# Kernel optimization log

Hardware: AMD Instinct MI355X
Metric: run time of the kernel (lower is better)

Reference implementation:

```python
import jax, jax.numpy as jnp
import numpy as np

NUM_EDGES = 10000
NUM_PATHS = 30000
MAX_LEN = 16
LINK_DIM = 128
PATH_DIM = 128


def setup_inputs() -> dict:
    key = jax.random.key(0)
    k0, k1, k2, k3, k4, k5, k6, k7 = jax.random.split(key, 8)
    inputs = jax.random.normal(k0, (NUM_EDGES, LINK_DIM), dtype=jnp.float32)
    # every path has exactly MAX_LEN hops -> unique (path, pos) scatter indices
    idx = jnp.repeat(jnp.arange(NUM_PATHS, dtype=jnp.int64), MAX_LEN)
    seqs = jnp.tile(jnp.arange(MAX_LEN, dtype=jnp.int64), NUM_PATHS)
    paths = jax.random.randint(k1, (NUM_PATHS * MAX_LEN,), 0, NUM_EDGES).astype(jnp.int64)
    # GRU params (Keras GRUCell, reset_after=True): kernel [D,3U], recurrent [U,3U], two bias rows
    s_in = 1.0 / np.sqrt(LINK_DIM)
    s_h = 1.0 / np.sqrt(PATH_DIM)
    kernel = jax.random.uniform(k2, (LINK_DIM, 3 * PATH_DIM), minval=-s_in, maxval=s_in, dtype=jnp.float32)
    rec_kernel = jax.random.uniform(k3, (PATH_DIM, 3 * PATH_DIM), minval=-s_h, maxval=s_h, dtype=jnp.float32)
    bias_i = jnp.zeros((3 * PATH_DIM,), dtype=jnp.float32)
    bias_r = jnp.zeros((3 * PATH_DIM,), dtype=jnp.float32)
    wq = jax.random.uniform(k4, (PATH_DIM, PATH_DIM), minval=-s_h, maxval=s_h, dtype=jnp.float32)
    wk = jax.random.uniform(k5, (PATH_DIM, PATH_DIM), minval=-s_h, maxval=s_h, dtype=jnp.float32)
    wv = jax.random.uniform(k6, (PATH_DIM, PATH_DIM), minval=-s_h, maxval=s_h, dtype=jnp.float32)
    return {"inputs": inputs, "paths": paths, "idx": idx, "seqs": seqs,
            "kernel": kernel, "rec_kernel": rec_kernel, "bias_i": bias_i, "bias_r": bias_r,
            "wq": wq, "wk": wk, "wv": wv}


def _gru_scan(link_inputs, kernel, rec_kernel, bias_i, bias_r):
    # link_inputs: [P, L, D] -> hidden_states [P, L, U], last_state [P, U]
    U = rec_kernel.shape[0]
    P = link_inputs.shape[0]
    xs = jnp.transpose(link_inputs, (1, 0, 2))  # [L, P, D]

    def step(h, x):
        xm = x @ kernel + bias_i          # [P, 3U]
        hm = h @ rec_kernel + bias_r      # [P, 3U]  (reset_after=True)
        xz, xr, xh = xm[:, :U], xm[:, U:2 * U], xm[:, 2 * U:]
        hz, hr, hh = hm[:, :U], hm[:, U:2 * U], hm[:, 2 * U:]
        z = jax.nn.sigmoid(xz + hz)
        r = jax.nn.sigmoid(xr + hr)
        cand = jnp.tanh(xh + r * hh)
        h_new = z * h + (1.0 - z) * cand
        return h_new, h_new

    h0 = jnp.zeros((P, U), dtype=link_inputs.dtype)
    last, hs = jax.lax.scan(step, h0, xs)
    return jnp.transpose(hs, (1, 0, 2)), last  # [P, L, U], [P, U]


def reference(inputs, paths, idx, seqs, kernel, rec_kernel, bias_i, bias_r, wq, wk, wv):
    h_tild = inputs[paths]  # gather: [P*L, D]
    link_inputs = jnp.zeros((NUM_PATHS, MAX_LEN, LINK_DIM), dtype=inputs.dtype)
    link_inputs = link_inputs.at[idx, seqs].set(h_tild)  # scatter_nd
    hidden_states, last_state = _gru_scan(link_inputs, kernel, rec_kernel, bias_i, bias_r)
    key = jnp.einsum('plu,uv->plv', hidden_states, wk)
    query = last_state @ wq                     # [P, U]
    value = jnp.einsum('plu,uv->plv', hidden_states, wv)
    att = jnp.einsum('plv,pv->pl', key, query)  # raw scores, no softmax (faithful)
    context = jnp.einsum('pl,plv->pv', att, value)[:, None, :]  # [P, 1, U]
    return context
```

## Files before the change

kernel.cpp:

```cpp
#include <hip/hip_runtime.h>


#define NUM_PATHS 30000
#define T 16
#define NTILES 1875
#define NPAIRS 938
#define NEDGES 10000

typedef float f32x4 __attribute__((ext_vector_type(4)));
typedef short bf16x8 __attribute__((ext_vector_type(8)));

__device__ __forceinline__ short f2bf(float f) {
    union { float f; unsigned u; } v; v.f = f;
    return (short)((v.u + 0x8000u) >> 16);
}
__device__ __forceinline__ float bf2f(short s) {
    union { unsigned u; float f; } v; v.u = ((unsigned)(unsigned short)s) << 16;
    return v.f;
}
__device__ __forceinline__ float fsig(float x) {
    return __builtin_amdgcn_rcpf(1.0f + __expf(-x));
}
__device__ __forceinline__ float ftanhf_(float x) {
    return 1.0f - 2.0f * __builtin_amdgcn_rcpf(1.0f + __expf(2.0f * x));
}

#define MFMA(a, b, c) __builtin_amdgcn_mfma_f32_16x16x32_bf16((a), (b), (c), 0, 0, 0)

#define GRU_T 12288
#define QK_T 16384
#define WV_T 2048
__global__ void prep_kernel(const float* __restrict__ Wx, const float* __restrict__ Wr,
                            const float* __restrict__ wq, const float* __restrict__ wk,
                            const float* __restrict__ wv,
                            short* __restrict__ wpk) {
    int id = blockIdx.x * 256 + threadIdx.x;
    if (id < GRU_T) {
        int f = id >> 9, rem = id & 511;
        int w = rem >> 6, lane = rem & 63;
        int quad = lane >> 4, c16 = lane & 15;
        int col = 16 * w + c16;
        short o[8];
        #pragma unroll
        for (int j = 0; j < 8; ++j) {
            float v;
            if (f < 16) {
                int k = (f & 7) * 32 + quad * 8 + j;
                int cc = col + ((f < 8) ? 0 : 128);
                v = (k < 128) ? Wx[k * 384 + cc] : Wr[(k - 128) * 384 + cc];
            } else {
                int k = ((f - 16) & 3) * 32 + quad * 8 + j;
                v = (f < 20) ? Wx[k * 384 + 256 + col] : Wr[k * 384 + 256 + col];
            }
            o[j] = f2bf(v);
        }
        *(bf16x8*)&wpk[id * 8] = *(bf16x8*)o;
        return;
    }
    if (id < GRU_T + QK_T) {
        int t2 = id - GRU_T;
        int j = t2 & 7, lane = (t2 >> 3) & 63, w = (t2 >> 9) & 7, kc = t2 >> 12;
        int quad = lane >> 4, c16 = lane & 15, col = 16 * w + c16;
        int k = kc * 32 + quad * 8 + j;
        const float* qr = wq + k * 128;
        const float* kr = wk + col * 128;
        float s = 0.f;
        #pragma unroll 8
        for (int vv = 0; vv < 128; ++vv) s += qr[vv] * kr[vv];
        short hi = f2bf(s);
        wpk[(((24 + kc) * 8 + w) * 64 + lane) * 8 + j] = hi;
        wpk[(((28 + kc) * 8 + w) * 64 + lane) * 8 + j] = f2bf(s - bf2f(hi));
        return;
    }
    if (id < GRU_T + QK_T + WV_T) {
        int t2 = id - GRU_T - QK_T;
        int lane = t2 & 63, w = (t2 >> 6) & 7, kc = t2 >> 9;
        int quad = lane >> 4, c16 = lane & 15, col = 16 * w + c16;
        short hi8[8], lo8[8];
        #pragma unroll
        for (int j = 0; j < 8; ++j) {
            float v = wv[(kc * 32 + quad * 8 + j) * 128 + col];
            hi8[j] = f2bf(v);
            lo8[j] = f2bf(v - bf2f(hi8[j]));
        }
        *(bf16x8*)&wpk[(((32 + kc) * 8 + w) * 64 + lane) * 8] = *(bf16x8*)hi8;
        *(bf16x8*)&wpk[(((36 + kc) * 8 + w) * 64 + lane) * 8] = *(bf16x8*)lo8;
    }
}

__global__ __launch_bounds__(512) void eprep_kernel(
    const float* __restrict__ inputs, const short* __restrict__ wpk,
    uint2* __restrict__ E8) {
    const int w = threadIdx.x >> 6, lane = threadIdx.x & 63;
    const int quad = lane >> 4, c16 = lane & 15;
    const int ucol = 16 * w + c16;
    const int e0 = blockIdx.x * 16;

    bf16x8 A[4];
    const float* row = inputs + (e0 + c16) * 128;
    #pragma unroll
    for (int kc = 0; kc < 4; ++kc) {
        float4 a = *(const float4*)&row[kc * 32 + quad * 8];
        float4 b = *(const float4*)&row[kc * 32 + quad * 8 + 4];
        short o[8] = {f2bf(a.x), f2bf(a.y), f2bf(a.z), f2bf(a.w),
                      f2bf(b.x), f2bf(b.y), f2bf(b.z), f2bf(b.w)};
        A[kc] = *(bf16x8*)o;
    }
    f32x4 az = {0.f, 0.f, 0.f, 0.f}, ar = az, ax = az;
    #pragma unroll
    for (int kc = 0; kc < 4; ++kc) {
        bf16x8 Bz = *(const bf16x8*)&wpk[(((0 + kc) * 8 + w) * 64 + lane) * 8];
        bf16x8 Br = *(const bf16x8*)&wpk[(((8 + kc) * 8 + w) * 64 + lane) * 8];
        bf16x8 Bx = *(const bf16x8*)&wpk[(((16 + kc) * 8 + w) * 64 + lane) * 8];
        az = MFMA(A[kc], Bz, az);
        ar = MFMA(A[kc], Br, ar);
        ax = MFMA(A[kc], Bx, ax);
    }
    #pragma unroll
    for (int r = 0; r < 4; ++r) {
        unsigned zr = (unsigned)(unsigned short)f2bf(az[r]) |
                      ((unsigned)(unsigned short)f2bf(ar[r]) << 16);
        uint2 val;
        val.x = zr;
        val.y = __float_as_uint(ax[r]);
        E8[(e0 + quad * 4 + r) * 128 + ucol] = val;
    }
}

#define ROWS 136
#define HSLOT 2184

__global__ __launch_bounds__(512, 2) void path_emb_kernel(
    const int* __restrict__ paths, const short* __restrict__ wpk,
    const uint2* __restrict__ E8,
    const float* __restrict__ bias_i, const float* __restrict__ bias_r,
    float* __restrict__ out)
{
    __shared__ __align__(16) short s_hist[2][16][HSLOT];
    __shared__ __align__(16) short s_xb[2][2][T * ROWS];
    __shared__ float s_att[2][16][20];

    const int tid  = threadIdx.x;
    const int w    = tid >> 6;
    const int lane = tid & 63;
    const int quad = lane >> 4;
    const int c16  = lane & 15;
    const int ucol = 16 * w + c16;

    const float bz  = bias_i[ucol] + bias_r[ucol];
    const float brr = bias_i[128 + ucol] + bias_r[128 + ucol];
    const float bxh = bias_i[256 + ucol];
    const float bhh = bias_r[256 + ucol];

    bf16x8 Bzh[4], Brh[4], Bhh[4];
    #pragma unroll
    for (int kc = 0; kc < 4; ++kc) {
        Bzh[kc] = *(const bf16x8*)&wpk[(((4 + kc)  * 8 + w) * 64 + lane) * 8];
        Brh[kc] = *(const bf16x8*)&wpk[(((12 + kc) * 8 + w) * 64 + lane) * 8];
        Bhh[kc] = *(const bf16x8*)&wpk[(((20 + kc) * 8 + w) * 64 + lane) * 8];
    }

    for (int pi = blockIdx.x; pi < NPAIRS; pi += gridDim.x) {
        const int tA = 2 * pi;
        const int tB = (2 * pi + 1 < NTILES) ? 2 * pi + 1 : NTILES - 1;
        const int p0A = tA * T, p0B = tB * T;

        float hA[4] = {0.f, 0.f, 0.f, 0.f}, hB[4] = {0.f, 0.f, 0.f, 0.f};

        uint2 Ea[8], Eb[8];
        {
            int e0i[8];
            #pragma unroll
            for (int i = 0; i < 4; ++i) {
                e0i[i]     = paths[(p0A + quad * 4 + i) * 16];
                e0i[4 + i] = paths[(p0B + quad * 4 + i) * 16];
            }
            #pragma unroll
            for (int i = 0; i < 8; ++i) Ea[i] = E8[e0i[i] * 128 + ucol];
        }

        auto window = [&](int t, uint2* Ecur, uint2* Enext) {
            __syncthreads();

            if (t < 15) {
                int en[8];
                #pragma unroll
                for (int i = 0; i < 4; ++i) {
                    en[i]     = paths[(p0A + quad * 4 + i) * 16 + t + 1];
                    en[4 + i] = paths[(p0B + quad * 4 + i) * 16 + t + 1];
                }
                #pragma unroll
                for (int i = 0; i < 8; ++i) Enext[i] = E8[en[i] * 128 + ucol];
            }

            f32x4 azA = {bz, bz, bz, bz},     azB = azA;
            f32x4 arA = {brr, brr, brr, brr}, arB = arA;
            f32x4 achA = {bhh, bhh, bhh, bhh}, achB = achA;

            if (t > 0) {
                bf16x8 ahA[4], ahB[4];
                #pragma unroll
                for (int kc = 0; kc < 4; ++kc) {
                    ahA[kc] = *(const bf16x8*)&s_hist[0][t - 1][c16 * ROWS + kc * 32 + quad * 8];
                    ahB[kc] = *(const bf16x8*)&s_hist[1][t - 1][c16 * ROWS + kc * 32 + quad * 8];
                }
                #pragma unroll
                for (int kc = 0; kc < 4; ++kc) {
                    azA  = MFMA(ahA[kc], Bzh[kc], azA);
                    azB  = MFMA(ahB[kc], Bzh[kc], azB);
                    arA  = MFMA(ahA[kc], Brh[kc], arA);
                    arB  = MFMA(ahB[kc], Brh[kc], arB);
                    achA = MFMA(ahA[kc], Bhh[kc], achA);
                    achB = MFMA(ahB[kc], Bhh[kc], achB);
                }
            }

            #pragma unroll
            for (int r = 0; r < 4; ++r) {
                float zx = __uint_as_float(Ecur[r].x << 16);
                float rx = __uint_as_float(Ecur[r].x & 0xffff0000u);
                float xh = __uint_as_float(Ecur[r].y);
                float z    = fsig(azA[r] + zx);
                float rr   = fsig(arA[r] + rx);
                float cand = ftanhf_(xh + bxh + rr * achA[r]);
                hA[r] = cand + z * (hA[r] - cand);
                s_hist[0][t][(quad * 4 + r) * ROWS + ucol] = f2bf(hA[r]);
            }
            #pragma unroll
            for (int r = 0; r < 4; ++r) {
                float zx = __uint_as_float(Ecur[4 + r].x << 16);
                float rx = __uint_as_float(Ecur[4 + r].x & 0xffff0000u);
                float xh = __uint_as_float(Ecur[4 + r].y);
                float z    = fsig(azB[r] + zx);
                float rr   = fsig(arB[r] + rx);
                float cand = ftanhf_(xh + bxh + rr * achB[r]);
                hB[r] = cand + z * (hB[r] - cand);
                s_hist[1][t][(quad * 4 + r) * ROWS + ucol] = f2bf(hB[r]);
            }
        };

        #pragma unroll 1
        for (int t2 = 0; t2 < 8; ++t2) {
            window(2 * t2,     Ea, Eb);
            window(2 * t2 + 1, Eb, Ea);
        }

        #pragma unroll
        for (int r = 0; r < 4; ++r) {
            float hf = hA[r]; short hi = f2bf(hf);
            s_xb[0][0][(quad * 4 + r) * ROWS + ucol] = f2bf(hf - bf2f(hi));
            hf = hB[r]; hi = f2bf(hf);
            s_xb[1][0][(quad * 4 + r) * ROWS + ucol] = f2bf(hf - bf2f(hi));
        }
        __syncthreads();

        f32x4 uA = {0.f, 0.f, 0.f, 0.f}, uB = uA;
        #pragma unroll
        for (int kc = 0; kc < 4; ++kc) {
            bf16x8 bqh = *(const bf16x8*)&wpk[(((24 + kc) * 8 + w) * 64 + lane) * 8];
            bf16x8 bql = *(const bf16x8*)&wpk[(((28 + kc) * 8 + w) * 64 + lane) * 8];
            bf16x8 AhA = *(const bf16x8*)&s_hist[0][15][c16 * ROWS + kc * 32 + quad * 8];
            bf16x8 AlA = *(const bf16x8*)&s_xb[0][0][c16 * ROWS + kc * 32 + quad * 8];
            bf16x8 AhB = *(const bf16x8*)&s_hist[1][15][c16 * ROWS + kc * 32 + quad * 8];
            bf16x8 AlB = *(const bf16x8*)&s_xb[1][0][c16 * ROWS + kc * 32 + quad * 8];
            uA = MFMA(AhA, bqh, uA); uA = MFMA(AhA, bql, uA); uA = MFMA(AlA, bqh, uA);
            uB = MFMA(AhB, bqh, uB); uB = MFMA(AhB, bql, uB); uB = MFMA(AlB, bqh, uB);
        }
        __syncthreads();

        #pragma unroll
        for (int r = 0; r < 4; ++r) {
            int off = (quad * 4 + r) * ROWS + ucol;
            float v = uA[r]; short hi = f2bf(v);
            s_xb[0][0][off] = hi; s_xb[0][1][off] = f2bf(v - bf2f(hi));
            v = uB[r]; hi = f2bf(v);
            s_xb[1][0][off] = hi; s_xb[1][1][off] = f2bf(v - bf2f(hi));
        }
        __syncthreads();

        {
            int et = tid >> 8, p = (tid >> 4) & 15, l = tid & 15;
            const short* uh = &s_xb[et][0][p * ROWS];
            const short* ul = &s_xb[et][1][p * ROWS];
            const short* hh = &s_hist[et][l][p * ROWS];
            float a = 0.f;
            #pragma unroll
            for (int u8 = 0; u8 < 128; u8 += 8) {
                bf16x8 vh = *(const bf16x8*)&uh[u8];
                bf16x8 vl = *(const bf16x8*)&ul[u8];
                bf16x8 vt = *(const bf16x8*)&hh[u8];
                #pragma unroll
                for (int j = 0; j < 8; ++j)
                    a += (bf2f(vh[j]) + bf2f(vl[j])) * bf2f(vt[j]);
            }
            s_att[et][p][l] = a;
        }
        __syncthreads();

        {
            int et = tid >> 8, p = (tid >> 4) & 15, v0 = (tid & 15) * 8;
            float ctx[8];
            #pragma unroll
            for (int j = 0; j < 8; ++j) ctx[j] = 0.f;
            #pragma unroll
            for (int l = 0; l < 16; ++l) {
                float al = s_att[et][p][l];
                bf16x8 hv = *(const bf16x8*)&s_hist[et][l][p * ROWS + v0];
                #pragma unroll
                for (int j = 0; j < 8; ++j) ctx[j] += al * bf2f(hv[j]);
            }
            #pragma unroll
            for (int j = 0; j < 8; ++j) {
                short hi = f2bf(ctx[j]);
                s_xb[et][0][p * ROWS + v0 + j] = hi;
                s_xb[et][1][p * ROWS + v0 + j] = f2bf(ctx[j] - bf2f(hi));
            }
        }
        __syncthreads();

        f32x4 oA = {0.f, 0.f, 0.f, 0.f}, oB = oA;
        #pragma unroll
        for (int kc = 0; kc < 4; ++kc) {
            bf16x8 bwh = *(const bf16x8*)&wpk[(((32 + kc) * 8 + w) * 64 + lane) * 8];
            bf16x8 bwl = *(const bf16x8*)&wpk[(((36 + kc) * 8 + w) * 64 + lane) * 8];
            bf16x8 AhA = *(const bf16x8*)&s_xb[0][0][c16 * ROWS + kc * 32 + quad * 8];
            bf16x8 AlA = *(const bf16x8*)&s_xb[0][1][c16 * ROWS + kc * 32 + quad * 8];
            bf16x8 AhB = *(const bf16x8*)&s_xb[1][0][c16 * ROWS + kc * 32 + quad * 8];
            bf16x8 AlB = *(const bf16x8*)&s_xb[1][1][c16 * ROWS + kc * 32 + quad * 8];
            oA = MFMA(AhA, bwh, oA); oA = MFMA(AhA, bwl, oA); oA = MFMA(AlA, bwh, oA);
            oB = MFMA(AhB, bwh, oB); oB = MFMA(AhB, bwl, oB); oB = MFMA(AlB, bwh, oB);
        }
        #pragma unroll
        for (int r = 0; r < 4; ++r) {
            out[(p0A + quad * 4 + r) * 128 + ucol] = oA[r];
            out[(p0B + quad * 4 + r) * 128 + ucol] = oB[r];
        }
    }
}

extern "C" void kernel_launch(void* const* d_in, const int* in_sizes, int n_in,
                              void* d_out, int out_size, void* d_ws, size_t ws_size,
                              hipStream_t stream) {
    const float* inputs = (const float*)d_in[0];
    const int*   paths  = (const int*)d_in[1];
    const float* wx  = (const float*)d_in[4];
    const float* wr  = (const float*)d_in[5];
    const float* bi  = (const float*)d_in[6];
    const float* br  = (const float*)d_in[7];
    const float* wq  = (const float*)d_in[8];
    const float* wk  = (const float*)d_in[9];
    const float* wvp = (const float*)d_in[10];

    char* ws = (char*)d_ws;
    uint2* E8 = (uint2*)ws;
    short* wpk = (short*)(ws + 10240000);

    int prep_n = GRU_T + QK_T + WV_T;
    prep_kernel<<<(prep_n + 255) / 256, 256, 0, stream>>>(wx, wr, wq, wk, wvp, wpk);
    eprep_kernel<<<NEDGES / 16, 512, 0, stream>>>(inputs, wpk, E8);
    path_emb_kernel<<<256, 512, 0, stream>>>(paths, wpk, E8, bi, br, (float*)d_out);
}
```

Baseline: 221.0 us.

## Process one 16-path tile per block and raise occupancy to four blocks per CU

```diff
diff --git a/kernel.cpp b/kernel.cpp
--- a/kernel.cpp
+++ b/kernel.cpp
@@ -4,11 +4,11 @@
 #define NUM_PATHS 30000
 #define T 16
 #define NTILES 1875
-#define NPAIRS 938
 #define NEDGES 10000
 
 typedef float f32x4 __attribute__((ext_vector_type(4)));
 typedef short bf16x8 __attribute__((ext_vector_type(8)));
+typedef short bf16x4 __attribute__((ext_vector_type(4)));
 
 __device__ __forceinline__ short f2bf(float f) {
     union { float f; unsigned u; } v; v.f = f;
@@ -130,14 +130,14 @@
 #define ROWS 136
 #define HSLOT 2184
 
-__global__ __launch_bounds__(512, 2) void path_emb_kernel(
+__global__ __launch_bounds__(512, 4) void path_emb_kernel(
     const int* __restrict__ paths, const short* __restrict__ wpk,
     const uint2* __restrict__ E8,
     const float* __restrict__ bias_i, const float* __restrict__ bias_r,
     float* __restrict__ out)
 {
-    __shared__ __align__(16) short s_hist[2][16][HSLOT];
-    __shared__ __align__(16) short s_xb[2][2][T * ROWS];
+    __shared__ __align__(16) short s_hist[16][HSLOT];
+    __shared__ __align__(16) short s_xb[2][T * ROWS];
     __shared__ float s_att[2][16][20];
 
     const int tid  = threadIdx.x;
@@ -160,182 +160,144 @@
         Bhh[kc] = *(const bf16x8*)&wpk[(((20 + kc) * 8 + w) * 64 + lane) * 8];
     }
 
-    for (int pi = blockIdx.x; pi < NPAIRS; pi += gridDim.x) {
-        const int tA = 2 * pi;
-        const int tB = (2 * pi + 1 < NTILES) ? 2 * pi + 1 : NTILES - 1;
-        const int p0A = tA * T, p0B = tB * T;
-
-        float hA[4] = {0.f, 0.f, 0.f, 0.f}, hB[4] = {0.f, 0.f, 0.f, 0.f};
-
-        uint2 Ea[8], Eb[8];
-        {
-            int e0i[8];
-            #pragma unroll
-            for (int i = 0; i < 4; ++i) {
-                e0i[i]     = paths[(p0A + quad * 4 + i) * 16];
-                e0i[4 + i] = paths[(p0B + quad * 4 + i) * 16];
+    const int p0 = blockIdx.x * T;
+
+    float hA[4] = {0.f, 0.f, 0.f, 0.f};
+
+    uint2 Ea[4], Eb[4];
+    {
+        int e0i[4];
+        #pragma unroll
+        for (int i = 0; i < 4; ++i)
+            e0i[i] = paths[(p0 + quad * 4 + i) * 16];
+        #pragma unroll
+        for (int i = 0; i < 4; ++i) Ea[i] = E8[e0i[i] * 128 + ucol];
+    }
+
+    auto window = [&](int t, uint2* Ecur, uint2* Enext) {
+        __syncthreads();
+
+        if (t < 15) {
+            int en[4];
+            #pragma unroll
+            for (int i = 0; i < 4; ++i)
+                en[i] = paths[(p0 + quad * 4 + i) * 16 + t + 1];
+            #pragma unroll
+            for (int i = 0; i < 4; ++i) Enext[i] = E8[en[i] * 128 + ucol];
+        }
+
+        f32x4 az  = {bz, bz, bz, bz};
+        f32x4 ar  = {brr, brr, brr, brr};
+        f32x4 ach = {bhh, bhh, bhh, bhh};
+
+        if (t > 0) {
+            bf16x8 ah[4];
+            #pragma unroll
+            for (int kc = 0; kc < 4; ++kc)
+                ah[kc] = *(const bf16x8*)&s_hist[t - 1][c16 * ROWS + kc * 32 + quad * 8];
+            #pragma unroll
+            for (int kc = 0; kc < 4; ++kc) {
+                az  = MFMA(ah[kc], Bzh[kc], az);
+                ar  = MFMA(ah[kc], Brh[kc], ar);
+                ach = MFMA(ah[kc], Bhh[kc], ach);
             }
-            #pragma unroll
-            for (int i = 0; i < 8; ++i) Ea[i] = E8[e0i[i] * 128 + ucol];
-        }
-
-        auto window = [&](int t, uint2* Ecur, uint2* Enext) {
-            __syncthreads();
-
-            if (t < 15) {
-                int en[8];
-                #pragma unroll
-                for (int i = 0; i < 4; ++i) {
-                    en[i]     = paths[(p0A + quad * 4 + i) * 16 + t + 1];
-                    en[4 + i] = paths[(p0B + quad * 4 + i) * 16 + t + 1];
-                }
-                #pragma unroll
-                for (int i = 0; i < 8; ++i) Enext[i] = E8[en[i] * 128 + ucol];
-            }
-
-            f32x4 azA = {bz, bz, bz, bz},     azB = azA;
-            f32x4 arA = {brr, brr, brr, brr}, arB = arA;
-            f32x4 achA = {bhh, bhh, bhh, bhh}, achB = achA;
-
-            if (t > 0) {
-                bf16x8 ahA[4], ahB[4];
-                #pragma unroll
-                for (int kc = 0; kc < 4; ++kc) {
-                    ahA[kc] = *(const bf16x8*)&s_hist[0][t - 1][c16 * ROWS + kc * 32 + quad * 8];
-                    ahB[kc] = *(const bf16x8*)&s_hist[1][t - 1][c16 * ROWS + kc * 32 + quad * 8];
-                }
-                #pragma unroll
-                for (int kc = 0; kc < 4; ++kc) {
-                    azA  = MFMA(ahA[kc], Bzh[kc], azA);
-                    azB  = MFMA(ahB[kc], Bzh[kc], azB);
-                    arA  = MFMA(ahA[kc], Brh[kc], arA);
-                    arB  = MFMA(ahB[kc], Brh[kc], arB);
-                    achA = MFMA(ahA[kc], Bhh[kc], achA);
-                    achB = MFMA(ahB[kc], Bhh[kc], achB);
-                }
-            }
-
-            #pragma unroll
-            for (int r = 0; r < 4; ++r) {
-                float zx = __uint_as_float(Ecur[r].x << 16);
-                float rx = __uint_as_float(Ecur[r].x & 0xffff0000u);
-                float xh = __uint_as_float(Ecur[r].y);
-                float z    = fsig(azA[r] + zx);
-                float rr   = fsig(arA[r] + rx);
-                float cand = ftanhf_(xh + bxh + rr * achA[r]);
-                hA[r] = cand + z * (hA[r] - cand);
-                s_hist[0][t][(quad * 4 + r) * ROWS + ucol] = f2bf(hA[r]);
-            }
-            #pragma unroll
-            for (int r = 0; r < 4; ++r) {
-                float zx = __uint_as_float(Ecur[4 + r].x << 16);
-                float rx = __uint_as_float(Ecur[4 + r].x & 0xffff0000u);
-                float xh = __uint_as_float(Ecur[4 + r].y);
-                float z    = fsig(azB[r] + zx);
-                float rr   = fsig(arB[r] + rx);
-                float cand = ftanhf_(xh + bxh + rr * achB[r]);
-                hB[r] = cand + z * (hB[r] - cand);
-                s_hist[1][t][(quad * 4 + r) * ROWS + ucol] = f2bf(hB[r]);
-            }
-        };
-
-        #pragma unroll 1
-        for (int t2 = 0; t2 < 8; ++t2) {
-            window(2 * t2,     Ea, Eb);
-            window(2 * t2 + 1, Eb, Ea);
         }
 
         #pragma unroll
         for (int r = 0; r < 4; ++r) {
-            float hf = hA[r]; short hi = f2bf(hf);
-            s_xb[0][0][(quad * 4 + r) * ROWS + ucol] = f2bf(hf - bf2f(hi));
-            hf = hB[r]; hi = f2bf(hf);
-            s_xb[1][0][(quad * 4 + r) * ROWS + ucol] = f2bf(hf - bf2f(hi));
-        }
-        __syncthreads();
-
-        f32x4 uA = {0.f, 0.f, 0.f, 0.f}, uB = uA;
-        #pragma unroll
-        for (int kc = 0; kc < 4; ++kc) {
-            bf16x8 bqh = *(const bf16x8*)&wpk[(((24 + kc) * 8 + w) * 64 + lane) * 8];
-            bf16x8 bql = *(const bf16x8*)&wpk[(((28 + kc) * 8 + w) * 64 + lane) * 8];
-            bf16x8 AhA = *(const bf16x8*)&s_hist[0][15][c16 * ROWS + kc * 32 + quad * 8];
-            bf16x8 AlA = *(const bf16x8*)&s_xb[0][0][c16 * ROWS + kc * 32 + quad * 8];
-            bf16x8 AhB = *(const bf16x8*)&s_hist[1][15][c16 * ROWS + kc * 32 + quad * 8];
-            bf16x8 AlB = *(const bf16x8*)&s_xb[1][0][c16 * ROWS + kc * 32 + quad * 8];
-            uA = MFMA(AhA, bqh, uA); uA = MFMA(AhA, bql, uA); uA = MFMA(AlA, bqh, uA);
-            uB = MFMA(AhB, bqh, uB); uB = MFMA(AhB, bql, uB); uB = MFMA(AlB, bqh, uB);
-        }
-        __syncthreads();
-
-        #pragma unroll
-        for (int r = 0; r < 4; ++r) {
-            int off = (quad * 4 + r) * ROWS + ucol;
-            float v = uA[r]; short hi = f2bf(v);
-            s_xb[0][0][off] = hi; s_xb[0][1][off] = f2bf(v - bf2f(hi));
-            v = uB[r]; hi = f2bf(v);
-            s_xb[1][0][off] = hi; s_xb[1][1][off] = f2bf(v - bf2f(hi));
-        }
-        __syncthreads();
-
-        {
-            int et = tid >> 8, p = (tid >> 4) & 15, l = tid & 15;
-            const short* uh = &s_xb[et][0][p * ROWS];
-            const short* ul = &s_xb[et][1][p * ROWS];
-            const short* hh = &s_hist[et][l][p * ROWS];
-            float a = 0.f;
-            #pragma unroll
-            for (int u8 = 0; u8 < 128; u8 += 8) {
-                bf16x8 vh = *(const bf16x8*)&uh[u8];
-                bf16x8 vl = *(const bf16x8*)&ul[u8];
-                bf16x8 vt = *(const bf16x8*)&hh[u8];
-                #pragma unroll
-                for (int j = 0; j < 8; ++j)
-                    a += (bf2f(vh[j]) + bf2f(vl[j])) * bf2f(vt[j]);
-            }
-            s_att[et][p][l] = a;
-        }
-        __syncthreads();
-
-        {
-            int et = tid >> 8, p = (tid >> 4) & 15, v0 = (tid & 15) * 8;
-            float ctx[8];
-            #pragma unroll
-            for (int j = 0; j < 8; ++j) ctx[j] = 0.f;
-            #pragma unroll
-            for (int l = 0; l < 16; ++l) {
-                float al = s_att[et][p][l];
-                bf16x8 hv = *(const bf16x8*)&s_hist[et][l][p * ROWS + v0];
-                #pragma unroll
-                for (int j = 0; j < 8; ++j) ctx[j] += al * bf2f(hv[j]);
-            }
-            #pragma unroll
-            for (int j = 0; j < 8; ++j) {
-                short hi = f2bf(ctx[j]);
-                s_xb[et][0][p * ROWS + v0 + j] = hi;
-                s_xb[et][1][p * ROWS + v0 + j] = f2bf(ctx[j] - bf2f(hi));
-            }
-        }
-        __syncthreads();
-
-        f32x4 oA = {0.f, 0.f, 0.f, 0.f}, oB = oA;
-        #pragma unroll
-        for (int kc = 0; kc < 4; ++kc) {
-            bf16x8 bwh = *(const bf16x8*)&wpk[(((32 + kc) * 8 + w) * 64 + lane) * 8];
-            bf16x8 bwl = *(const bf16x8*)&wpk[(((36 + kc) * 8 + w) * 64 + lane) * 8];
-            bf16x8 AhA = *(const bf16x8*)&s_xb[0][0][c16 * ROWS + kc * 32 + quad * 8];
-            bf16x8 AlA = *(const bf16x8*)&s_xb[0][1][c16 * ROWS + kc * 32 + quad * 8];
-            bf16x8 AhB = *(const bf16x8*)&s_xb[1][0][c16 * ROWS + kc * 32 + quad * 8];
-            bf16x8 AlB = *(const bf16x8*)&s_xb[1][1][c16 * ROWS + kc * 32 + quad * 8];
-            oA = MFMA(AhA, bwh, oA); oA = MFMA(AhA, bwl, oA); oA = MFMA(AlA, bwh, oA);
-            oB = MFMA(AhB, bwh, oB); oB = MFMA(AhB, bwl, oB); oB = MFMA(AlB, bwh, oB);
-        }
-        #pragma unroll
-        for (int r = 0; r < 4; ++r) {
-            out[(p0A + quad * 4 + r) * 128 + ucol] = oA[r];
-            out[(p0B + quad * 4 + r) * 128 + ucol] = oB[r];
-        }
-    }
+            float zx = __uint_as_float(Ecur[r].x << 16);
+            float rx = __uint_as_float(Ecur[r].x & 0xffff0000u);
+            float xh = __uint_as_float(Ecur[r].y);
+            float z    = fsig(az[r] + zx);
+            float rr   = fsig(ar[r] + rx);
+            float cand = ftanhf_(xh + bxh + rr * ach[r]);
+            hA[r] = cand + z * (hA[r] - cand);
+            s_hist[t][(quad * 4 + r) * ROWS + ucol] = f2bf(hA[r]);
+        }
+    };
+
+    #pragma unroll 1
+    for (int t2 = 0; t2 < 8; ++t2) {
+        window(2 * t2,     Ea, Eb);
+        window(2 * t2 + 1, Eb, Ea);
+    }
+
+    #pragma unroll
+    for (int r = 0; r < 4; ++r) {
+        float hf = hA[r]; short hi = f2bf(hf);
+        s_xb[0][(quad * 4 + r) * ROWS + ucol] = f2bf(hf - bf2f(hi));
+    }
+    __syncthreads();
+
+    f32x4 uA = {0.f, 0.f, 0.f, 0.f};
+    #pragma unroll
+    for (int kc = 0; kc < 4; ++kc) {
+        bf16x8 bqh = *(const bf16x8*)&wpk[(((24 + kc) * 8 + w) * 64 + lane) * 8];
+        bf16x8 bql = *(const bf16x8*)&wpk[(((28 + kc) * 8 + w) * 64 + lane) * 8];
+        bf16x8 Ah  = *(const bf16x8*)&s_hist[15][c16 * ROWS + kc * 32 + quad * 8];
+        bf16x8 Al  = *(const bf16x8*)&s_xb[0][c16 * ROWS + kc * 32 + quad * 8];
+        uA = MFMA(Ah, bqh, uA); uA = MFMA(Ah, bql, uA); uA = MFMA(Al, bqh, uA);
+    }
+    __syncthreads();
+
+    #pragma unroll
+    for (int r = 0; r < 4; ++r) {
+        int off = (quad * 4 + r) * ROWS + ucol;
+        float v = uA[r]; short hi = f2bf(v);
+        s_xb[0][off] = hi; s_xb[1][off] = f2bf(v - bf2f(hi));
+    }
+    __syncthreads();
+
+    {
+        int half = tid >> 8, p = (tid >> 4) & 15, l = tid & 15;
+        const short* uh = &s_xb[0][p * ROWS + half * 64];
+        const short* ul = &s_xb[1][p * ROWS + half * 64];
+        const short* hh = &s_hist[l][p * ROWS + half * 64];
+        float a = 0.f;
+        #pragma unroll
+        for (int u8 = 0; u8 < 64; u8 += 8) {
+            bf16x8 vh = *(const bf16x8*)&uh[u8];
+            bf16x8 vl = *(const bf16x8*)&ul[u8];
+            bf16x8 vt = *(const bf16x8*)&hh[u8];
+            #pragma unroll
+            for (int j = 0; j < 8; ++j)
+                a += (bf2f(vh[j]) + bf2f(vl[j])) * bf2f(vt[j]);
+        }
+        s_att[half][p][l] = a;
+    }
+    __syncthreads();
+
+    {
+        int p = tid >> 5, c0 = (tid & 31) * 4;
+        float ctx[4] = {0.f, 0.f, 0.f, 0.f};
+        #pragma unroll
+        for (int l = 0; l < 16; ++l) {
+            float al = s_att[0][p][l] + s_att[1][p][l];
+            bf16x4 hv = *(const bf16x4*)&s_hist[l][p * ROWS + c0];
+            #pragma unroll
+            for (int j = 0; j < 4; ++j) ctx[j] += al * bf2f(hv[j]);
+        }
+        #pragma unroll
+        for (int j = 0; j < 4; ++j) {
+            short hi = f2bf(ctx[j]);
+            s_xb[0][p * ROWS + c0 + j] = hi;
+            s_xb[1][p * ROWS + c0 + j] = f2bf(ctx[j] - bf2f(hi));
+        }
+    }
+    __syncthreads();
+
+    f32x4 oA = {0.f, 0.f, 0.f, 0.f};
+    #pragma unroll
+    for (int kc = 0; kc < 4; ++kc) {
+        bf16x8 bwh = *(const bf16x8*)&wpk[(((32 + kc) * 8 + w) * 64 + lane) * 8];
+        bf16x8 bwl = *(const bf16x8*)&wpk[(((36 + kc) * 8 + w) * 64 + lane) * 8];
+        bf16x8 Ah  = *(const bf16x8*)&s_xb[0][c16 * ROWS + kc * 32 + quad * 8];
+        bf16x8 Al  = *(const bf16x8*)&s_xb[1][c16 * ROWS + kc * 32 + quad * 8];
+        oA = MFMA(Ah, bwh, oA); oA = MFMA(Ah, bwl, oA); oA = MFMA(Al, bwh, oA);
+    }
+    #pragma unroll
+    for (int r = 0; r < 4; ++r)
+        out[(p0 + quad * 4 + r) * 128 + ucol] = oA[r];
 }
 
 extern "C" void kernel_launch(void* const* d_in, const int* in_sizes, int n_in,
@@ -358,5 +320,5 @@
     int prep_n = GRU_T + QK_T + WV_T;
     prep_kernel<<<(prep_n + 255) / 256, 256, 0, stream>>>(wx, wr, wq, wk, wvp, wpk);
     eprep_kernel<<<NEDGES / 16, 512, 0, stream>>>(inputs, wpk, E8);
-    path_emb_kernel<<<256, 512, 0, stream>>>(paths, wpk, E8, bi, br, (float*)d_out);
-}
+    path_emb_kernel<<<NTILES, 512, 0, stream>>>(paths, wpk, E8, bi, br, (float*)d_out);
+}
```

New measurement: 208.9 us. -5.5%, faster.
